# Kernel optimization log

Measured on AMD Instinct MI355X. Metric: run time of the kernel, lower is better.

The kernel has to match this reference:

```python
import jax, jax.numpy as jnp
import numpy as np

N_NODES = 50000
N_EDGES = 400000
HID = 256
NUM_LAYERS = 2
NUM_LEVELS = 8  # depth of the constructed leveled DAG


def _build_dag_edges():
    # Leveled DAG: NUM_LEVELS levels of equal size; every edge goes from
    # level l (src) to level l+1 (dst), guaranteeing termination in
    # exactly NUM_LEVELS topological sweeps.
    rng = np.random.default_rng(0)
    per_level = N_NODES // NUM_LEVELS
    dst_level = rng.integers(1, NUM_LEVELS, size=N_EDGES)
    dst = dst_level * per_level + rng.integers(0, per_level, size=N_EDGES)
    src = (dst_level - 1) * per_level + rng.integers(0, per_level, size=N_EDGES)
    return jnp.asarray(np.stack([src, dst]).astype(np.int32))


def setup_inputs() -> dict:
    key = jax.random.key(0)
    ks = jax.random.split(key, 8)
    s = 0.05
    V = jax.random.normal(ks[0], (N_NODES, HID), dtype=jnp.float32)
    E = _build_dag_edges()
    dense_w = jax.random.normal(ks[1], (HID, HID), dtype=jnp.float32) * s
    dense_b = jax.random.normal(ks[2], (HID,), dtype=jnp.float32) * s
    gru_w_ih = jax.random.normal(ks[3], (NUM_LAYERS, 3 * HID, HID), dtype=jnp.float32) * s
    gru_w_hh = jax.random.normal(ks[4], (NUM_LAYERS, 3 * HID, HID), dtype=jnp.float32) * s
    gru_b_ih = jax.random.normal(ks[5], (NUM_LAYERS, 3 * HID), dtype=jnp.float32) * s
    gru_b_hh = jax.random.normal(ks[6], (NUM_LAYERS, 3 * HID), dtype=jnp.float32) * s
    return {"V": V, "E": E, "dense_w": dense_w, "dense_b": dense_b,
            "gru_w_ih": gru_w_ih, "gru_w_hh": gru_w_hh,
            "gru_b_ih": gru_b_ih, "gru_b_hh": gru_b_hh}


def _gru_cell(x, h, w_ih, w_hh, b_ih, b_hh):
    gi = x @ w_ih.T + b_ih
    gh = h @ w_hh.T + b_hh
    i_r, i_z, i_n = jnp.split(gi, 3, axis=-1)
    h_r, h_z, h_n = jnp.split(gh, 3, axis=-1)
    r = jax.nn.sigmoid(i_r + h_r)
    z = jax.nn.sigmoid(i_z + h_z)
    n = jnp.tanh(i_n + r * h_n)
    return (1.0 - z) * n + z * h


def _dag_gru_layer(x, src, dst, w_ih, w_hh, b_ih, b_hh):
    N = x.shape[0]
    H = w_hh.shape[1]

    def step(carry, _):
        hidden, avail = carry
        # nodes that are dst of an edge whose source is still available
        blocked = jnp.zeros((N,), dtype=bool).at[dst].max(avail[src])
        leaf = avail & ~blocked
        use = leaf[dst]  # edges feeding a leaf node this sweep
        msgs = jnp.where(use[:, None], hidden[src], 0.0)  # [E, H]
        agg = jax.ops.segment_sum(msgs, dst, num_segments=N)  # [N, H]
        new_h = _gru_cell(x, agg, w_ih, w_hh, b_ih, b_hh)
        hidden = jnp.where(leaf[:, None], new_h, hidden)
        return (hidden, avail & ~leaf), None

    init = (jnp.zeros((N, H), dtype=x.dtype), jnp.ones((N,), dtype=bool))
    (hidden, _), _ = jax.lax.scan(step, init, None, length=NUM_LEVELS)
    return hidden


def reference(V, E, dense_w, dense_b, gru_w_ih, gru_w_hh, gru_b_ih, gru_b_hh):
    src, dst = E[0], E[1]
    hidden = V @ dense_w.T + dense_b
    for l in range(NUM_LAYERS):
        hidden = _dag_gru_layer(hidden, src, dst,
                                gru_w_ih[l], gru_w_hh[l],
                                gru_b_ih[l], gru_b_hh[l])
    return hidden
```

## Files before the change

### kernel.cpp

```cpp
#include <hip/hip_runtime.h>

#define HID 256
#define NSTEPS 8

typedef __attribute__((ext_vector_type(4))) float f32x4;
typedef __attribute__((ext_vector_type(8))) short s16x8;
typedef __attribute__((ext_vector_type(4))) short s16x4;

__device__ __forceinline__ unsigned short f2bf(float f) {
  unsigned u = __builtin_bit_cast(unsigned, f);
  u += 0x7fffu + ((u >> 16) & 1u);
  return (unsigned short)(u >> 16);
}
__device__ __forceinline__ float bf2f(unsigned short s) {
  return __builtin_bit_cast(float, ((unsigned)s) << 16);
}

__device__ __forceinline__ f32x4 mfma16(s16x8 a, s16x8 b, f32x4 c) {
  return __builtin_amdgcn_mfma_f32_16x16x32_bf16(a, b, c, 0, 0, 0);
}

__device__ __forceinline__ void split3(const float* p, s16x8& a0, s16x8& a1, s16x8& a2) {
  f32x4 u = *(const f32x4*)p;
  f32x4 v = *(const f32x4*)(p + 4);
  float f[8] = {u[0], u[1], u[2], u[3], v[0], v[1], v[2], v[3]};
#pragma unroll
  for (int j = 0; j < 8; ++j) {
    unsigned short l0 = f2bf(f[j]);
    float r1 = f[j] - bf2f(l0);
    unsigned short l1 = f2bf(r1);
    float r2 = r1 - bf2f(l1);
    a0[j] = (short)l0;
    a1[j] = (short)l1;
    a2[j] = (short)f2bf(r2);
  }
}


__global__ void k_limb(const float* __restrict__ in, short* __restrict__ o0,
                       short* __restrict__ o1, short* __restrict__ o2, int n) {
  int i = blockIdx.x * 256 + threadIdx.x;
  if (i < n) {
    float x = in[i];
    unsigned short l0 = f2bf(x);
    float r1 = x - bf2f(l0);
    unsigned short l1 = f2bf(r1);
    o0[i] = (short)l0;
    o1[i] = (short)l1;
    o2[i] = (short)f2bf(r1 - bf2f(l1));
  }
}


__global__ void k_indeg(const int* __restrict__ dst, int* __restrict__ indeg, int E) {
  int e = blockIdx.x * blockDim.x + threadIdx.x;
  if (e < E) atomicAdd(&indeg[dst[e]], 1);
}

__global__ void k_blocksum(const int* __restrict__ indeg, int* __restrict__ bsum, int N) {
  __shared__ int s[256];
  int i = blockIdx.x * 256 + threadIdx.x;
  s[threadIdx.x] = (i < N) ? indeg[i] : 0;
  __syncthreads();
  for (int st = 128; st > 0; st >>= 1) {
    if (threadIdx.x < st) s[threadIdx.x] += s[threadIdx.x + st];
    __syncthreads();
  }
  if (threadIdx.x == 0) bsum[blockIdx.x] = s[0];
}

__global__ void k_bscan(const int* __restrict__ bsum, int* __restrict__ boff,
                        int NB, int* __restrict__ total) {
  if (threadIdx.x == 0 && blockIdx.x == 0) {
    int a = 0;
    for (int i = 0; i < NB; ++i) { boff[i] = a; a += bsum[i]; }
    *total = a;
  }
}

__global__ void k_scan3(const int* __restrict__ indeg, const int* __restrict__ boff,
                        int* __restrict__ csr_off, int N) {
  __shared__ int s[256];
  int tx = threadIdx.x;
  int i = blockIdx.x * 256 + tx;
  int v = (i < N) ? indeg[i] : 0;
  s[tx] = v;
  __syncthreads();
  for (int st = 1; st < 256; st <<= 1) {
    int t = (tx >= st) ? s[tx - st] : 0;
    __syncthreads();
    s[tx] += t;
    __syncthreads();
  }
  if (i < N) csr_off[i] = boff[blockIdx.x] + s[tx] - v;
}

__global__ void k_fill(const int* __restrict__ src, const int* __restrict__ dst,
                       const int* __restrict__ csr_off, int* __restrict__ cursor,
                       int* __restrict__ csr_src, int E) {
  int e = blockIdx.x * blockDim.x + threadIdx.x;
  if (e < E) {
    int d = dst[e];
    int p = atomicAdd(&cursor[d], 1);
    csr_src[csr_off[d] + p] = src[e];
  }
}


__global__ void k_aggf2(const float* __restrict__ HA, const float* __restrict__ HB,
                        int t, int PB,
                        const int* __restrict__ csr_off, const int* __restrict__ csr_src,
                        float* __restrict__ aggFA, float* __restrict__ aggFB,
                        short* __restrict__ GA0, short* __restrict__ GA1,
                        short* __restrict__ GA2,
                        short* __restrict__ GB0, short* __restrict__ GB1,
                        short* __restrict__ GB2) {
  const int z = blockIdx.z;
  const int s = t - z;
  if (s < 0 || s >= NSTEPS) return;
  const float* H = z ? HB : HA;
  float* aggF = z ? aggFB : aggFA;
  short* G0 = z ? GB0 : GA0;
  short* G1 = z ? GB1 : GA1;
  short* G2 = z ? GB2 : GA2;

  const int grp = threadIdx.x >> 6, lane = threadIdx.x & 63;
  const int r = blockIdx.x * 4 + grp;
  if (r >= PB) return;
  const int node = s * PB + r;
  const int b = csr_off[node], e = csr_off[node + 1];
  const int c4 = lane * 4;
  f32x4 acc = (f32x4){0.f, 0.f, 0.f, 0.f};
  for (int j = b; j < e; ++j) {
    f32x4 v = *(const f32x4*)&H[(size_t)csr_src[j] * HID + c4];
    acc[0] += v[0]; acc[1] += v[1]; acc[2] += v[2]; acc[3] += v[3];
  }
  size_t o = (size_t)r * HID + c4;
  *(f32x4*)&aggF[o] = acc;
  s16x4 g0, g1, g2;
#pragma unroll
  for (int q = 0; q < 4; ++q) {
    unsigned short l0 = f2bf(acc[q]);
    float r1 = acc[q] - bf2f(l0);
    unsigned short l1 = f2bf(r1);
    g0[q] = (short)l0;
    g1[q] = (short)l1;
    g2[q] = (short)f2bf(r1 - bf2f(l1));
  }
  *(s16x4*)&G0[o] = g0;
  *(s16x4*)&G1[o] = g1;
  *(s16x4*)&G2[o] = g2;
}

__global__ __launch_bounds__(256, 2)
void k_dense8(const float* __restrict__ V, const short* __restrict__ dwS,
              const float* __restrict__ db,
              short* __restrict__ A0, short* __restrict__ A1,
              short* __restrict__ A2, int M) {
  __shared__ s16x8 lds[2][24 * 64];
  const int tid = threadIdx.x;
  const int w = tid >> 6, lane = tid & 63;
  const int lr = lane & 15, lg = lane >> 4;
  const int c0 = blockIdx.x * 128;
  const int m0 = blockIdx.y * 64 + w * 16;
  const float* xrow = V + (size_t)min(m0 + lr, M - 1) * HID;

  const short* sp[6];
  int so[6];
#pragma unroll
  for (int q = 0; q < 6; ++q) {
    int f = w * 6 + q;
    int a = f >> 3, t = f & 7;
    sp[q] = dwS + a * (HID * HID) + (size_t)(c0 + t * 16 + lr) * HID + lg * 8;
    so[q] = f * 64 + lane;
  }

  s16x8 rr[6];
#pragma unroll
  for (int q = 0; q < 6; ++q) rr[q] = *(const s16x8*)(sp[q]);
#pragma unroll
  for (int q = 0; q < 6; ++q) lds[0][so[q]] = rr[q];

  f32x4 acc[8];
#pragma unroll
  for (int t = 0; t < 8; ++t) acc[t] = (f32x4){0.f, 0.f, 0.f, 0.f};

  for (int kc = 0; kc < 8; ++kc) {
    if (kc < 7) {
#pragma unroll
      for (int q = 0; q < 6; ++q) rr[q] = *(const s16x8*)(sp[q] + (kc + 1) * 32);
    }
    __syncthreads();
    const s16x8* buf = lds[kc & 1];
    int kb = kc * 32 + lg * 8;
    s16x8 x0, x1, x2;
    split3(xrow + kb, x0, x1, x2);
#pragma unroll
    for (int t = 0; t < 8; ++t) {
      s16x8 w0f = buf[(0 * 8 + t) * 64 + lane];
      s16x8 w1f = buf[(1 * 8 + t) * 64 + lane];
      s16x8 w2f = buf[(2 * 8 + t) * 64 + lane];
      f32x4 a = acc[t];
      a = mfma16(x0, w0f, a);
      a = mfma16(x0, w1f, a);
      a = mfma16(x1, w0f, a);
      a = mfma16(x1, w1f, a);
      a = mfma16(x0, w2f, a);
      a = mfma16(x2, w0f, a);
      acc[t] = a;
    }
    if (kc < 7) {
#pragma unroll
      for (int q = 0; q < 6; ++q) lds[(kc + 1) & 1][so[q]] = rr[q];
    }
  }

#pragma unroll
  for (int t = 0; t < 8; ++t) {
    int col = c0 + t * 16 + lr;
    float bb = db[col];
#pragma unroll
    for (int r = 0; r < 4; ++r) {
      int row = m0 + lg * 4 + r;
      if (row < M) {
        float v = acc[t][r] + bb;
        unsigned short l0 = f2bf(v);
        float r1 = v - bf2f(l0);
        unsigned short l1 = f2bf(r1);
        size_t o = (size_t)row * HID + col;
        A0[o] = (short)l0;
        A1[o] = (short)l1;
        A2[o] = (short)f2bf(r1 - bf2f(l1));
      }
    }
  }
}

__global__ __launch_bounds__(512, 2)
void k_stepP(const short* __restrict__ A0, const short* __restrict__ A1,
             const short* __restrict__ A2,
             const short* __restrict__ B0, const short* __restrict__ B1,
             const short* __restrict__ B2,
             const short* __restrict__ GA0, const short* __restrict__ GA1,
             const short* __restrict__ GA2,
             const short* __restrict__ GB0, const short* __restrict__ GB1,
             const short* __restrict__ GB2,
             const float* __restrict__ aggFA, const float* __restrict__ aggFB,
             const short* __restrict__ wS,
             const float* __restrict__ b_ih, const float* __restrict__ b_hh,
             int t, int PB, float* __restrict__ Bfp, float* __restrict__ outp) {
  const int z = blockIdx.z;
  const int s = t - z;
  if (s < 0 || s >= NSTEPS) return;

  const short* X0 = z ? B0 : A0;
  const short* X1 = z ? B1 : A1;
  const short* X2 = z ? B2 : A2;
  const short* G0 = z ? GB0 : GA0;
  const short* G1 = z ? GB1 : GA1;
  const short* G2 = z ? GB2 : GA2;
  const float* aggF = z ? aggFB : aggFA;
  const int AS = 768 * HID;
  const short* wSL = wS + (size_t)z * 6 * AS;
  const float* bi = b_ih + z * 768;
  const float* bh = b_hh + z * 768;
  float* Hf = z ? outp : Bfp;
  const bool outl = (z == 0);

  __shared__ s16x8 lds[8][18][64];
  const int tid = threadIdx.x;
  const int w = tid >> 6, lane = tid & 63;
  const int lr = lane & 15, lg = lane >> 4;
  const int c0 = blockIdx.x * 16;
  const int nb = s * PB;

  for (int u = w; u < 144; u += 8) {
    int f = u >> 3, kc = u & 7;
    int a = f / 3, g = f - a * 3;
    const short* srcp = wSL + (size_t)a * AS + (size_t)(g * HID + c0 + lr) * HID + kc * 32 + lg * 8;
    lds[kc][f][lane] = *(const s16x8*)srcp;
  }
  __syncthreads();

  for (int m0b = blockIdx.y * 256; m0b < PB; m0b += 256 * gridDim.y) {
    const int m0w = m0b + w * 32;
    int rowA[2];
    rowA[0] = min(m0w + lr, PB - 1);
    rowA[1] = min(m0w + 16 + lr, PB - 1);

    f32x4 acci[3][2], acch[3][2];
#pragma unroll
    for (int g = 0; g < 3; ++g)
#pragma unroll
      for (int rg = 0; rg < 2; ++rg) {
        acci[g][rg] = (f32x4){0.f, 0.f, 0.f, 0.f};
        acch[g][rg] = (f32x4){0.f, 0.f, 0.f, 0.f};
      }

    for (int kc = 0; kc < 8; ++kc) {
      const int kb = kc * 32 + lg * 8;
      s16x8 x0[2], x1[2], x2[2], g0[2], g1[2], g2[2];
#pragma unroll
      for (int rg = 0; rg < 2; ++rg) {
        size_t xb = (size_t)(nb + rowA[rg]) * HID + kb;
        x0[rg] = *(const s16x8*)&X0[xb];
        x1[rg] = *(const s16x8*)&X1[xb];
        x2[rg] = *(const s16x8*)&X2[xb];
        size_t gb = (size_t)rowA[rg] * HID + kb;
        g0[rg] = *(const s16x8*)&G0[gb];
        g1[rg] = *(const s16x8*)&G1[gb];
        g2[rg] = *(const s16x8*)&G2[gb];
      }
#pragma unroll
      for (int g = 0; g < 3; ++g) {
        s16x8 wi0f = lds[kc][0 * 3 + g][lane];
        s16x8 wi1f = lds[kc][1 * 3 + g][lane];
        s16x8 wi2f = lds[kc][2 * 3 + g][lane];
        s16x8 wh0f = lds[kc][3 * 3 + g][lane];
        s16x8 wh1f = lds[kc][4 * 3 + g][lane];
        s16x8 wh2f = lds[kc][5 * 3 + g][lane];
#pragma unroll
        for (int rg = 0; rg < 2; ++rg) {
          f32x4 a = acci[g][rg];
          a = mfma16(x0[rg], wi0f, a);
          a = mfma16(x0[rg], wi1f, a);
          a = mfma16(x1[rg], wi0f, a);
          a = mfma16(x1[rg], wi1f, a);
          a = mfma16(x0[rg], wi2f, a);
          a = mfma16(x2[rg], wi0f, a);
          acci[g][rg] = a;
          f32x4 h = acch[g][rg];
          h = mfma16(g0[rg], wh0f, h);
          h = mfma16(g0[rg], wh1f, h);
          h = mfma16(g1[rg], wh0f, h);
          h = mfma16(g1[rg], wh1f, h);
          h = mfma16(g0[rg], wh2f, h);
          h = mfma16(g2[rg], wh0f, h);
          acch[g][rg] = h;
        }
      }
    }

    {
      int col = c0 + lr;
      float bir = bi[col], biz = bi[HID + col], bin = bi[2 * HID + col];
      float bhr = bh[col], bhz = bh[HID + col], bhn = bh[2 * HID + col];
#pragma unroll
      for (int rg = 0; rg < 2; ++rg) {
#pragma unroll
        for (int r = 0; r < 4; ++r) {
          int row = m0w + rg * 16 + lg * 4 + r;
          if (row < PB) {
            float ir = acci[0][rg][r] + bir;
            float iz = acci[1][rg][r] + biz;
            float in_ = acci[2][rg][r] + bin;
            float hr = acch[0][rg][r] + bhr;
            float hz = acch[1][rg][r] + bhz;
            float hn = acch[2][rg][r] + bhn;
            float rgate = 1.f / (1.f + expf(-(ir + hr)));
            float zg = 1.f / (1.f + expf(-(iz + hz)));
            float ng = tanhf(in_ + rgate * hn);
            float a = aggF[(size_t)row * HID + col];
            float h = (1.f - zg) * ng + zg * a;
            size_t o = (size_t)(nb + row) * HID + col;
            Hf[o] = h;
            if (outl) {
              unsigned short l0 = f2bf(h);
              float r1 = h - bf2f(l0);
              unsigned short l1 = f2bf(r1);
              ((short*)B0)[o] = (short)l0;
              ((short*)B1)[o] = (short)l1;
              ((short*)B2)[o] = (short)f2bf(r1 - bf2f(l1));
            }
          }
        }
      }
    }
  }
}


extern "C" void kernel_launch(void* const* d_in, const int* in_sizes, int n_in,
                              void* d_out, int out_size, void* d_ws, size_t ws_size,
                              hipStream_t stream) {
  const float* V = (const float*)d_in[0];
  const int* E = (const int*)d_in[1];
  const float* dense_w = (const float*)d_in[2];
  const float* dense_b = (const float*)d_in[3];
  const float* w_ih = (const float*)d_in[4];
  const float* w_hh = (const float*)d_in[5];
  const float* b_ih = (const float*)d_in[6];
  const float* b_hh = (const float*)d_in[7];
  const int N = in_sizes[0] / HID;
  const int Ecnt = in_sizes[1] / 2;
  const int PB = N / NSTEPS;
  const int* src = E;
  const int* dst = E + Ecnt;
  float* out = (float*)d_out;

  const size_t AS = (size_t)768 * HID;

  char* p = (char*)d_ws;
  short* A0 = (short*)p;    p += (size_t)N * HID * 2;
  short* A1 = (short*)p;    p += (size_t)N * HID * 2;
  short* A2 = (short*)p;    p += (size_t)N * HID * 2;
  float* B = (float*)p;     p += (size_t)N * HID * 4;
  short* B0 = (short*)p;    p += (size_t)N * HID * 2;
  short* B1 = (short*)p;    p += (size_t)N * HID * 2;
  short* B2 = (short*)p;    p += (size_t)N * HID * 2;
  float* aggFA = (float*)p; p += (size_t)PB * HID * 4;
  float* aggFB = (float*)p; p += (size_t)PB * HID * 4;
  short* GA0 = (short*)p;   p += (size_t)PB * HID * 2;
  short* GA1 = (short*)p;   p += (size_t)PB * HID * 2;
  short* GA2 = (short*)p;   p += (size_t)PB * HID * 2;
  short* GB0 = (short*)p;   p += (size_t)PB * HID * 2;
  short* GB1 = (short*)p;   p += (size_t)PB * HID * 2;
  short* GB2 = (short*)p;   p += (size_t)PB * HID * 2;
  short* dwS = (short*)p;   p += (size_t)3 * HID * HID * 2;
  short* wS = (short*)p;    p += (size_t)2 * 6 * AS * 2;
  int* indeg = (int*)p;     p += (size_t)N * 4;
  int* cursor = (int*)p;    p += (size_t)N * 4;
  int* csr_off = (int*)p;   p += (size_t)(N + 1) * 4;
  int* csr_src = (int*)p;   p += (size_t)Ecnt * 4;
  int* bsum = (int*)p;      p += 256 * 4;
  int* boff = (int*)p;      p += 256 * 4;

  hipMemsetAsync(indeg, 0, (size_t)2 * N * 4, stream);

  const int TB = 256;
  const int egrid = (Ecnt + TB - 1) / TB;
  const int NB = (N + 255) / 256;
  const int wgrid = ((int)AS + 255) / 256;

  k_limb<<<(HID * HID + 255) / 256, TB, 0, stream>>>(
      dense_w, dwS, dwS + HID * HID, dwS + 2 * HID * HID, HID * HID);
  for (int l = 0; l < 2; ++l) {
    k_limb<<<wgrid, TB, 0, stream>>>(w_ih + l * AS, wS + (l * 6 + 0) * AS,
                                     wS + (l * 6 + 1) * AS, wS + (l * 6 + 2) * AS, (int)AS);
    k_limb<<<wgrid, TB, 0, stream>>>(w_hh + l * AS, wS + (l * 6 + 3) * AS,
                                     wS + (l * 6 + 4) * AS, wS + (l * 6 + 5) * AS, (int)AS);
  }

  k_dense8<<<dim3(2, (N + 63) / 64), TB, 0, stream>>>(V, dwS, dense_b, A0, A1, A2, N);

  k_indeg<<<egrid, TB, 0, stream>>>(dst, indeg, Ecnt);
  k_blocksum<<<NB, TB, 0, stream>>>(indeg, bsum, N);
  k_bscan<<<1, 1, 0, stream>>>(bsum, boff, NB, csr_off + N);
  k_scan3<<<NB, TB, 0, stream>>>(indeg, boff, csr_off, N);
  k_fill<<<egrid, TB, 0, stream>>>(src, dst, csr_off, cursor, csr_src, Ecnt);

  const dim3 agrid((PB + 3) / 4, 1, 2);
  const dim3 sgrid(HID / 16, 8, 2);
  for (int t = 0; t <= NSTEPS; ++t) {
    k_aggf2<<<agrid, TB, 0, stream>>>(B, out, t, PB, csr_off, csr_src,
                                      aggFA, aggFB, GA0, GA1, GA2, GB0, GB1, GB2);
    k_stepP<<<sgrid, 512, 0, stream>>>(A0, A1, A2, B0, B1, B2,
                                       GA0, GA1, GA2, GB0, GB1, GB2,
                                       aggFA, aggFB, wS, b_ih, b_hh,
                                       t, PB, B, out);
  }
}
```

Measured before the change: 1.272 ms.

## Replace LDS-staged step GEMM with XCD-aware flat grid and direct weight loads

The per-step GRU GEMM kernel no longer stages weight fragments in shared memory and no longer loops over row tiles. It launches a flat 1D grid whose block index is decoded so that each XCD (block index mod 8) handles one layer and one row quarter. Each wave computes a single 16-row tile and reads weights straight from global memory, relying on L2 locality within each XCD. This removes the LDS staging and its barrier and raises parallelism, at the cost of more global weight traffic per block and a hardcoded grid size that must cover PB.

```diff
diff --git a/kernel.cpp b/kernel.cpp
--- a/kernel.cpp
+++ b/kernel.cpp
@@ -236,8 +236,8 @@
   }
 }
 
-__global__ __launch_bounds__(512, 2)
-void k_stepP(const short* __restrict__ A0, const short* __restrict__ A1,
+__global__ __launch_bounds__(512)
+void k_stepW(const short* __restrict__ A0, const short* __restrict__ A1,
              const short* __restrict__ A2,
              const short* __restrict__ B0, const short* __restrict__ B1,
              const short* __restrict__ B2,
@@ -249,7 +249,17 @@
              const short* __restrict__ wS,
              const float* __restrict__ b_ih, const float* __restrict__ b_hh,
              int t, int PB, float* __restrict__ Bfp, float* __restrict__ outp) {
-  const int z = blockIdx.z;
+  const int L = blockIdx.x;
+  const int xcd = L & 7;
+  const int sl = L >> 3;
+  const int z = xcd & 1;
+  const int mq = xcd >> 1;
+  const int cblk = sl & 15;
+  const int mk = sl >> 4;
+  const int mchunk = mq + 4 * mk;
+  const int nmch = (PB + 127) / 128;
+  if (mchunk >= nmch) return;
+
   const int s = t - z;
   if (s < 0 || s >= NSTEPS) return;
 
@@ -267,112 +277,87 @@
   float* Hf = z ? outp : Bfp;
   const bool outl = (z == 0);
 
-  __shared__ s16x8 lds[8][18][64];
   const int tid = threadIdx.x;
   const int w = tid >> 6, lane = tid & 63;
   const int lr = lane & 15, lg = lane >> 4;
-  const int c0 = blockIdx.x * 16;
+  const int c0 = cblk * 16;
   const int nb = s * PB;
-
-  for (int u = w; u < 144; u += 8) {
-    int f = u >> 3, kc = u & 7;
-    int a = f / 3, g = f - a * 3;
-    const short* srcp = wSL + (size_t)a * AS + (size_t)(g * HID + c0 + lr) * HID + kc * 32 + lg * 8;
-    lds[kc][f][lane] = *(const s16x8*)srcp;
-  }
-  __syncthreads();
-
-  for (int m0b = blockIdx.y * 256; m0b < PB; m0b += 256 * gridDim.y) {
-    const int m0w = m0b + w * 32;
-    int rowA[2];
-    rowA[0] = min(m0w + lr, PB - 1);
-    rowA[1] = min(m0w + 16 + lr, PB - 1);
-
-    f32x4 acci[3][2], acch[3][2];
-#pragma unroll
-    for (int g = 0; g < 3; ++g)
-#pragma unroll
-      for (int rg = 0; rg < 2; ++rg) {
-        acci[g][rg] = (f32x4){0.f, 0.f, 0.f, 0.f};
-        acch[g][rg] = (f32x4){0.f, 0.f, 0.f, 0.f};
-      }
-
-    for (int kc = 0; kc < 8; ++kc) {
-      const int kb = kc * 32 + lg * 8;
-      s16x8 x0[2], x1[2], x2[2], g0[2], g1[2], g2[2];
-#pragma unroll
-      for (int rg = 0; rg < 2; ++rg) {
-        size_t xb = (size_t)(nb + rowA[rg]) * HID + kb;
-        x0[rg] = *(const s16x8*)&X0[xb];
-        x1[rg] = *(const s16x8*)&X1[xb];
-        x2[rg] = *(const s16x8*)&X2[xb];
-        size_t gb = (size_t)rowA[rg] * HID + kb;
-        g0[rg] = *(const s16x8*)&G0[gb];
-        g1[rg] = *(const s16x8*)&G1[gb];
-        g2[rg] = *(const s16x8*)&G2[gb];
-      }
-#pragma unroll
-      for (int g = 0; g < 3; ++g) {
-        s16x8 wi0f = lds[kc][0 * 3 + g][lane];
-        s16x8 wi1f = lds[kc][1 * 3 + g][lane];
-        s16x8 wi2f = lds[kc][2 * 3 + g][lane];
-        s16x8 wh0f = lds[kc][3 * 3 + g][lane];
-        s16x8 wh1f = lds[kc][4 * 3 + g][lane];
-        s16x8 wh2f = lds[kc][5 * 3 + g][lane];
-#pragma unroll
-        for (int rg = 0; rg < 2; ++rg) {
-          f32x4 a = acci[g][rg];
-          a = mfma16(x0[rg], wi0f, a);
-          a = mfma16(x0[rg], wi1f, a);
-          a = mfma16(x1[rg], wi0f, a);
-          a = mfma16(x1[rg], wi1f, a);
-          a = mfma16(x0[rg], wi2f, a);
-          a = mfma16(x2[rg], wi0f, a);
-          acci[g][rg] = a;
-          f32x4 h = acch[g][rg];
-          h = mfma16(g0[rg], wh0f, h);
-          h = mfma16(g0[rg], wh1f, h);
-          h = mfma16(g1[rg], wh0f, h);
-          h = mfma16(g1[rg], wh1f, h);
-          h = mfma16(g0[rg], wh2f, h);
-          h = mfma16(g2[rg], wh0f, h);
-          acch[g][rg] = h;
-        }
-      }
-    }
-
-    {
-      int col = c0 + lr;
-      float bir = bi[col], biz = bi[HID + col], bin = bi[2 * HID + col];
-      float bhr = bh[col], bhz = bh[HID + col], bhn = bh[2 * HID + col];
-#pragma unroll
-      for (int rg = 0; rg < 2; ++rg) {
-#pragma unroll
-        for (int r = 0; r < 4; ++r) {
-          int row = m0w + rg * 16 + lg * 4 + r;
-          if (row < PB) {
-            float ir = acci[0][rg][r] + bir;
-            float iz = acci[1][rg][r] + biz;
-            float in_ = acci[2][rg][r] + bin;
-            float hr = acch[0][rg][r] + bhr;
-            float hz = acch[1][rg][r] + bhz;
-            float hn = acch[2][rg][r] + bhn;
-            float rgate = 1.f / (1.f + expf(-(ir + hr)));
-            float zg = 1.f / (1.f + expf(-(iz + hz)));
-            float ng = tanhf(in_ + rgate * hn);
-            float a = aggF[(size_t)row * HID + col];
-            float h = (1.f - zg) * ng + zg * a;
-            size_t o = (size_t)(nb + row) * HID + col;
-            Hf[o] = h;
-            if (outl) {
-              unsigned short l0 = f2bf(h);
-              float r1 = h - bf2f(l0);
-              unsigned short l1 = f2bf(r1);
-              ((short*)B0)[o] = (short)l0;
-              ((short*)B1)[o] = (short)l1;
-              ((short*)B2)[o] = (short)f2bf(r1 - bf2f(l1));
-            }
-          }
+  const int m0w = mchunk * 128 + w * 16;
+  const int rowA = min(m0w + lr, PB - 1);
+
+  f32x4 acci[3], acch[3];
+#pragma unroll
+  for (int g = 0; g < 3; ++g) {
+    acci[g] = (f32x4){0.f, 0.f, 0.f, 0.f};
+    acch[g] = (f32x4){0.f, 0.f, 0.f, 0.f};
+  }
+
+  for (int kc = 0; kc < 8; ++kc) {
+    const int kb = kc * 32 + lg * 8;
+    size_t xb = (size_t)(nb + rowA) * HID + kb;
+    s16x8 x0 = *(const s16x8*)&X0[xb];
+    s16x8 x1 = *(const s16x8*)&X1[xb];
+    s16x8 x2 = *(const s16x8*)&X2[xb];
+    size_t gb = (size_t)rowA * HID + kb;
+    s16x8 g0 = *(const s16x8*)&G0[gb];
+    s16x8 g1 = *(const s16x8*)&G1[gb];
+    s16x8 g2 = *(const s16x8*)&G2[gb];
+#pragma unroll
+    for (int g = 0; g < 3; ++g) {
+      size_t wo = (size_t)(g * HID + c0 + lr) * HID + kb;
+      s16x8 wi0f = *(const s16x8*)&wSL[0 * AS + wo];
+      s16x8 wi1f = *(const s16x8*)&wSL[1 * AS + wo];
+      s16x8 wi2f = *(const s16x8*)&wSL[2 * AS + wo];
+      s16x8 wh0f = *(const s16x8*)&wSL[3 * AS + wo];
+      s16x8 wh1f = *(const s16x8*)&wSL[4 * AS + wo];
+      s16x8 wh2f = *(const s16x8*)&wSL[5 * AS + wo];
+      f32x4 a = acci[g];
+      a = mfma16(x0, wi0f, a);
+      a = mfma16(x0, wi1f, a);
+      a = mfma16(x1, wi0f, a);
+      a = mfma16(x1, wi1f, a);
+      a = mfma16(x0, wi2f, a);
+      a = mfma16(x2, wi0f, a);
+      acci[g] = a;
+      f32x4 h = acch[g];
+      h = mfma16(g0, wh0f, h);
+      h = mfma16(g0, wh1f, h);
+      h = mfma16(g1, wh0f, h);
+      h = mfma16(g1, wh1f, h);
+      h = mfma16(g0, wh2f, h);
+      h = mfma16(g2, wh0f, h);
+      acch[g] = h;
+    }
+  }
+
+  {
+    int col = c0 + lr;
+    float bir = bi[col], biz = bi[HID + col], bin = bi[2 * HID + col];
+    float bhr = bh[col], bhz = bh[HID + col], bhn = bh[2 * HID + col];
+#pragma unroll
+    for (int r = 0; r < 4; ++r) {
+      int row = m0w + lg * 4 + r;
+      if (row < PB) {
+        float ir = acci[0][r] + bir;
+        float iz = acci[1][r] + biz;
+        float in_ = acci[2][r] + bin;
+        float hr = acch[0][r] + bhr;
+        float hz = acch[1][r] + bhz;
+        float hn = acch[2][r] + bhn;
+        float rgate = 1.f / (1.f + expf(-(ir + hr)));
+        float zg = 1.f / (1.f + expf(-(iz + hz)));
+        float ng = tanhf(in_ + rgate * hn);
+        float a = aggF[(size_t)row * HID + col];
+        float h = (1.f - zg) * ng + zg * a;
+        size_t o = (size_t)(nb + row) * HID + col;
+        Hf[o] = h;
+        if (outl) {
+          unsigned short l0 = f2bf(h);
+          float r1 = h - bf2f(l0);
+          unsigned short l1 = f2bf(r1);
+          ((short*)B0)[o] = (short)l0;
+          ((short*)B1)[o] = (short)l1;
+          ((short*)B2)[o] = (short)f2bf(r1 - bf2f(l1));
         }
       }
     }
@@ -450,13 +435,13 @@
   k_fill<<<egrid, TB, 0, stream>>>(src, dst, csr_off, cursor, csr_src, Ecnt);
 
   const dim3 agrid((PB + 3) / 4, 1, 2);
-  const dim3 sgrid(HID / 16, 8, 2);
+  const int sblocks = 8 * 16 * 13;
   for (int t = 0; t <= NSTEPS; ++t) {
     k_aggf2<<<agrid, TB, 0, stream>>>(B, out, t, PB, csr_off, csr_src,
                                       aggFA, aggFB, GA0, GA1, GA2, GB0, GB1, GB2);
-    k_stepP<<<sgrid, 512, 0, stream>>>(A0, A1, A2, B0, B1, B2,
-                                       GA0, GA1, GA2, GB0, GB1, GB2,
-                                       aggFA, aggFB, wS, b_ih, b_hh,
-                                       t, PB, B, out);
-  }
-}
+    k_stepW<<<sblocks, 512, 0, stream>>>(A0, A1, A2, B0, B1, B2,
+                                         GA0, GA1, GA2, GB0, GB1, GB2,
+                                         aggFA, aggFB, wS, b_ih, b_hh,
+                                         t, PB, B, out);
+  }
+}
```

Measured after the change: 2.986 ms. 2.35x slower.
